# Performance work log

Hardware: AMD Instinct MI355X
Metric: run time of the kernel (lower is better)

The kernel has to match this reference:

```python
import jax, jax.numpy as jnp
import numpy as np

N, B, E = 10000, 4, 160000
C_IN, C_OUT, C_E = 64, 64, 16


def _mk_params(key, c_in, c_out, c_e):
    ks = jax.random.split(key, 8)
    s = 0.1
    return dict(
        w_n=jax.random.normal(ks[0], (c_in, c_out), jnp.float32) * s,
        w_e=jax.random.normal(ks[1], (c_e, c_out), jnp.float32) * s,
        q=jax.random.normal(ks[2], (c_out, c_out), jnp.float32) * s,
        k=jax.random.normal(ks[3], (c_out, c_out), jnp.float32) * s,
        aw=jax.random.normal(ks[4], (3 * c_out, 1), jnp.float32) * s,
        ab=jax.random.normal(ks[5], (1,), jnp.float32) * s,
        ow=jax.random.normal(ks[6], (2 * c_out, c_out), jnp.float32) * s,
        ob=jax.random.normal(ks[7], (c_out,), jnp.float32) * s,
    )


def setup_inputs() -> dict:
    key = jax.random.key(0)
    kx, ke, ka, k1, k2 = jax.random.split(key, 5)
    inp = {
        'X': jax.random.normal(kx, (N, B, C_IN), jnp.float32),
        'edge_index': jax.random.randint(ke, (2, E), 0, N, jnp.int32),
        'edge_attr': jax.random.normal(ka, (E, C_E), jnp.float32),
    }
    p1 = _mk_params(k1, C_IN, C_OUT, C_E)
    p2 = _mk_params(k2, C_OUT, C_OUT, C_E)
    for name, v in p1.items():
        inp[name + '1'] = v
    for name, v in p2.items():
        inp[name + '2'] = v
    return inp


def egnn_conv(x, edge_index, edge_attr, w_n, w_e, q, k, aw, ab, ow, ob, n_nodes):
    # x: [N,B,Cin]; edge_attr: [E,Ce]
    xp = x @ w_n                         # [N,B,C]
    ea = edge_attr @ w_e                 # [E,C]
    src, dst = edge_index[0], edge_index[1]
    xj = xp[src]                         # [E,B,C] gather (source)
    xi = xp[dst]                         # [E,B,C] gather (target)
    qf = xj @ q                          # [E,B,C]
    kf = xi @ k                          # [E,B,C]
    eab = jnp.broadcast_to(ea[:, None, :], qf.shape)  # [E,B,C]
    att_feat = jnp.concatenate([qf, kf, eab], axis=-1)  # [E,B,3C]
    att = jax.nn.sigmoid(att_feat @ aw + ab)            # [E,B,1]
    gate = jax.nn.sigmoid(eab)
    msg = att * xj * gate                # [E,B,C]
    aggr = jax.ops.segment_max(msg, dst, num_segments=n_nodes)  # [N,B,C]
    aggr = jnp.where(jnp.isneginf(aggr), 0.0, aggr)  # empty segments -> 0
    out = jnp.concatenate([xp, aggr], axis=-1) @ ow + ob
    return xp + out


def reference(X, edge_index, edge_attr,
              w_n1, w_e1, q1, k1, aw1, ab1, ow1, ob1,
              w_n2, w_e2, q2, k2, aw2, ab2, ow2, ob2):
    n_nodes = X.shape[0]
    c1 = egnn_conv(X, edge_index, edge_attr, w_n1, w_e1, q1, k1, aw1, ab1, ow1, ob1, n_nodes)
    c1 = jax.nn.leaky_relu(c1, 0.01)
    c2 = egnn_conv(c1, edge_index, edge_attr, w_n2, w_e2, q2, k2, aw2, ab2, ow2, ob2, n_nodes)
    c2 = jax.nn.leaky_relu(c2, 0.01)
    return c2
```

## Files before the change

### kernel.cpp

```cpp
#include <hip/hip_runtime.h>
#include <math.h>

#define NN 10000
#define BB 4
#define EE 160000
#define CC 64
#define CE 16

static constexpr size_t OFF_XPA    = 0;
static constexpr size_t OFF_XPB    = 10240000;
static constexpr size_t OFF_SA     = 20480000;
static constexpr size_t OFF_SB     = 20640000;
static constexpr size_t OFF_VECS   = 20800000;
static constexpr size_t OFF_COUNTS = 20801280;
static constexpr size_t OFF_CURSOR = 20841280;
static constexpr size_t OFF_OFFS   = 20881280;
static constexpr size_t OFF_RECS   = 20921344;
static constexpr size_t OFF_ATT    = 22201344;
static constexpr size_t OFF_SE12   = 24761344;
static constexpr size_t OFF_ORDER  = 26041344;

__device__ __forceinline__ float sigmoidf_(float x) {
    return __builtin_amdgcn_rcpf(1.0f + __expf(-x));
}

__global__ void hist_vecs_kernel(const int* __restrict__ ei, int* __restrict__ counts,
                                 const float* __restrict__ q1, const float* __restrict__ k1,
                                 const float* __restrict__ aw1, const float* __restrict__ we1,
                                 const float* __restrict__ q2, const float* __restrict__ k2,
                                 const float* __restrict__ aw2, const float* __restrict__ we2,
                                 float* __restrict__ vecs) {
    int e = blockIdx.x * blockDim.x + threadIdx.x;
    if (e < EE) atomicAdd(&counts[ei[EE + e]], 1);
    if (blockIdx.x == 0) {
        int t = threadIdx.x;
        if (t < 64) {
            float a = 0.f, b = 0.f, c = 0.f, d = 0.f;
            for (int j = 0; j < 64; ++j) {
                a = fmaf(q1[t * 64 + j], aw1[j], a);
                b = fmaf(k1[t * 64 + j], aw1[64 + j], b);
                c = fmaf(q2[t * 64 + j], aw2[j], c);
                d = fmaf(k2[t * 64 + j], aw2[64 + j], d);
            }
            vecs[t] = a; vecs[64 + t] = b; vecs[144 + t] = c; vecs[208 + t] = d;
        }
        if (t < 16) {
            float a = 0.f, b = 0.f;
            for (int j = 0; j < 64; ++j) {
                a = fmaf(we1[t * 64 + j], aw1[128 + j], a);
                b = fmaf(we2[t * 64 + j], aw2[128 + j], b);
            }
            vecs[128 + t] = a; vecs[272 + t] = b;
        }
    }
}

__global__ __launch_bounds__(1024) void scan_order_kernel(const int* __restrict__ counts,
                                                          int* __restrict__ offs,
                                                          int* __restrict__ order) {
    __shared__ int hist[1024];
    __shared__ int cur[1024];
    __shared__ int startb[1024];
    __shared__ int wsum[16];
    int t = threadIdx.x;
    hist[t] = 0; cur[t] = 0;
    int lane = t & 63, wid = t >> 6;
    int v[10];
    int s = 0;
    #pragma unroll
    for (int j = 0; j < 10; ++j) {
        int i = t * 10 + j;
        v[j] = (i < NN) ? counts[i] : 0;
        s += v[j];
    }
    int ps = s;
    #pragma unroll
    for (int off = 1; off < 64; off <<= 1) {
        int u = __shfl_up(ps, off, 64);
        if (lane >= off) ps += u;
    }
    if (lane == 63) wsum[wid] = ps;
    __syncthreads();
    int wbase = 0;
    for (int w = 0; w < wid; ++w) wbase += wsum[w];
    int tb = wbase + ps - s;
    #pragma unroll
    for (int j = 0; j < 10; ++j) {
        int i = t * 10 + j;
        if (i < NN) offs[i] = tb;
        tb += v[j];
    }
    if (t == 1023) offs[NN] = tb;
    #pragma unroll
    for (int j = 0; j < 10; ++j) {
        int i = t * 10 + j;
        if (i < NN) {
            int d = v[j] > 1023 ? 1023 : v[j];
            atomicAdd(&hist[d], 1);
        }
    }
    __syncthreads();
    int r = 1023 - t;
    int hv = hist[r];
    int ps2 = hv;
    #pragma unroll
    for (int off = 1; off < 64; off <<= 1) {
        int u = __shfl_up(ps2, off, 64);
        if (lane >= off) ps2 += u;
    }
    if (lane == 63) wsum[wid] = ps2;
    __syncthreads();
    int wb2 = 0;
    for (int w = 0; w < wid; ++w) wb2 += wsum[w];
    startb[r] = wb2 + ps2 - hv;
    __syncthreads();
    #pragma unroll
    for (int j = 0; j < 10; ++j) {
        int i = t * 10 + j;
        if (i < NN) {
            int d = v[j] > 1023 ? 1023 : v[j];
            int pos = startb[d] + atomicAdd(&cur[d], 1);
            order[pos] = i;
        }
    }
}

__global__ __launch_bounds__(256) void scatter_kernel(
    const int* __restrict__ ei, const int* __restrict__ offs,
    int* __restrict__ cursor, const float* __restrict__ attr,
    const float* __restrict__ vecs, const float* __restrict__ ab1,
    const float* __restrict__ ab2, int2* __restrict__ recs,
    float2* __restrict__ se12) {
    int e = blockIdx.x * blockDim.x + threadIdx.x;
    if (e >= EE) return;
    int s = ei[e], d = ei[EE + e];
    const float4* ap = (const float4*)(attr + (size_t)e * CE);
    float4 a0 = ap[0], a1 = ap[1], a2 = ap[2], a3 = ap[3];
    const float* v1 = vecs + 128;
    const float* v2 = vecs + 272;
    float s1 = ab1[0], s2 = ab2[0];
    s1 = fmaf(a0.x, v1[0], s1);  s1 = fmaf(a0.y, v1[1], s1);
    s1 = fmaf(a0.z, v1[2], s1);  s1 = fmaf(a0.w, v1[3], s1);
    s1 = fmaf(a1.x, v1[4], s1);  s1 = fmaf(a1.y, v1[5], s1);
    s1 = fmaf(a1.z, v1[6], s1);  s1 = fmaf(a1.w, v1[7], s1);
    s1 = fmaf(a2.x, v1[8], s1);  s1 = fmaf(a2.y, v1[9], s1);
    s1 = fmaf(a2.z, v1[10], s1); s1 = fmaf(a2.w, v1[11], s1);
    s1 = fmaf(a3.x, v1[12], s1); s1 = fmaf(a3.y, v1[13], s1);
    s1 = fmaf(a3.z, v1[14], s1); s1 = fmaf(a3.w, v1[15], s1);
    s2 = fmaf(a0.x, v2[0], s2);  s2 = fmaf(a0.y, v2[1], s2);
    s2 = fmaf(a0.z, v2[2], s2);  s2 = fmaf(a0.w, v2[3], s2);
    s2 = fmaf(a1.x, v2[4], s2);  s2 = fmaf(a1.y, v2[5], s2);
    s2 = fmaf(a1.z, v2[6], s2);  s2 = fmaf(a1.w, v2[7], s2);
    s2 = fmaf(a2.x, v2[8], s2);  s2 = fmaf(a2.y, v2[9], s2);
    s2 = fmaf(a2.z, v2[10], s2); s2 = fmaf(a2.w, v2[11], s2);
    s2 = fmaf(a3.x, v2[12], s2); s2 = fmaf(a3.y, v2[13], s2);
    s2 = fmaf(a3.z, v2[14], s2); s2 = fmaf(a3.w, v2[15], s2);
    int p = atomicAdd(&cursor[d], 1);
    recs[offs[d] + p] = make_int2(s, e);
    se12[e] = make_float2(s1, s2);
}

__global__ __launch_bounds__(256) void node_prep_kernel(
    const float* __restrict__ x, const float* __restrict__ w_n,
    const float* __restrict__ qa, const float* __restrict__ ka,
    float* __restrict__ xp, float* __restrict__ sa, float* __restrict__ sb) {
    __shared__ float w_sh[64 * 64];
    __shared__ float x_sh[4 * BB * CC];
    int t = threadIdx.x;
    for (int i = t; i < 64 * 64; i += 256) w_sh[i] = w_n[i];
    int node0 = blockIdx.x * 4;
    const float4* xg = (const float4*)(x + (size_t)node0 * BB * CC);
    ((float4*)x_sh)[t] = xg[t];
    __syncthreads();
    int wave = t >> 6, lane = t & 63;
    int node = node0 + wave;
    const float* xrow = x_sh + wave * BB * CC;
    float acc0 = 0.f, acc1 = 0.f, acc2 = 0.f, acc3 = 0.f;
    #pragma unroll 8
    for (int ci = 0; ci < 64; ++ci) {
        float w = w_sh[ci * 64 + lane];
        acc0 = fmaf(xrow[ci], w, acc0);
        acc1 = fmaf(xrow[64 + ci], w, acc1);
        acc2 = fmaf(xrow[128 + ci], w, acc2);
        acc3 = fmaf(xrow[192 + ci], w, acc3);
    }
    size_t obase = (size_t)node * BB * CC + lane;
    xp[obase] = acc0;
    xp[obase + 64] = acc1;
    xp[obase + 128] = acc2;
    xp[obase + 192] = acc3;
    float qv = qa[lane], kv = ka[lane];
    float ra0 = acc0 * qv, ra1 = acc1 * qv, ra2 = acc2 * qv, ra3 = acc3 * qv;
    float rb0 = acc0 * kv, rb1 = acc1 * kv, rb2 = acc2 * kv, rb3 = acc3 * kv;
    #pragma unroll
    for (int off = 32; off >= 1; off >>= 1) {
        ra0 += __shfl_xor(ra0, off, 64); ra1 += __shfl_xor(ra1, off, 64);
        ra2 += __shfl_xor(ra2, off, 64); ra3 += __shfl_xor(ra3, off, 64);
        rb0 += __shfl_xor(rb0, off, 64); rb1 += __shfl_xor(rb1, off, 64);
        rb2 += __shfl_xor(rb2, off, 64); rb3 += __shfl_xor(rb3, off, 64);
    }
    if (lane == 0) {
        sa[node * BB + 0] = ra0; sa[node * BB + 1] = ra1;
        sa[node * BB + 2] = ra2; sa[node * BB + 3] = ra3;
        sb[node * BB + 0] = rb0; sb[node * BB + 1] = rb1;
        sb[node * BB + 2] = rb2; sb[node * BB + 3] = rb3;
    }
}

__global__ __launch_bounds__(256) void att_kernel(
    const int* __restrict__ ei, const float2* __restrict__ se12,
    const float* __restrict__ sa, const float* __restrict__ sb,
    float4* __restrict__ att, int sel) {
    int e = blockIdx.x * blockDim.x + threadIdx.x;
    if (e >= EE) return;
    int s = ei[e], d = ei[EE + e];
    float2 se2 = se12[e];
    float se = sel ? se2.y : se2.x;
    float4 sas = *(const float4*)(sa + (size_t)s * BB);
    float4 sbn = *(const float4*)(sb + (size_t)d * BB);
    float4 r;
    r.x = sigmoidf_(sas.x + sbn.x + se);
    r.y = sigmoidf_(sas.y + sbn.y + se);
    r.z = sigmoidf_(sas.z + sbn.z + se);
    r.w = sigmoidf_(sas.w + sbn.w + se);
    att[e] = r;
}

#define FMA4(o_, s_, w_)                                                 \
    o_.x = fmaf(s_, w_.x, o_.x); o_.y = fmaf(s_, w_.y, o_.y);            \
    o_.z = fmaf(s_, w_.z, o_.z); o_.w = fmaf(s_, w_.w, o_.w);

__global__ __launch_bounds__(256) void conv_out_kernel(
    const float* __restrict__ xp,
    const int2* __restrict__ recs,
    const int* __restrict__ offs,
    const float* __restrict__ attr,
    const float* __restrict__ w_e,
    const float4* __restrict__ att,
    const float* __restrict__ ow,
    const float* __restrict__ ob,
    const int* __restrict__ order,
    float* __restrict__ out) {
    __shared__ float aggr_sh[4][BB * 68];
    int t = threadIdx.x;
    int wave = t >> 6, lane = t & 63;
    int node = order[blockIdx.x * 4 + wave];

    float wec[CE];
    #pragma unroll
    for (int j = 0; j < CE; ++j) wec[j] = w_e[j * CC + lane];

    int o0 = offs[node], o1 = offs[node + 1];
    float m0 = -INFINITY, m1 = -INFINITY, m2 = -INFINITY, m3 = -INFINITY;

    int i = o0;
    int2 rec = (i < o1) ? recs[i] : make_int2(0, 0);
    while (i < o1) {
        int2 cur = rec;
        ++i;
        if (i < o1) rec = recs[i];
        int s = cur.x, e = cur.y;
        float4 at = att[e];
        const float4* ap = (const float4*)(attr + (size_t)e * CE);
        float4 a0 = ap[0], a1 = ap[1], a2 = ap[2], a3 = ap[3];
        float g = 0.f;
        g = fmaf(a0.x, wec[0], g);  g = fmaf(a0.y, wec[1], g);
        g = fmaf(a0.z, wec[2], g);  g = fmaf(a0.w, wec[3], g);
        g = fmaf(a1.x, wec[4], g);  g = fmaf(a1.y, wec[5], g);
        g = fmaf(a1.z, wec[6], g);  g = fmaf(a1.w, wec[7], g);
        g = fmaf(a2.x, wec[8], g);  g = fmaf(a2.y, wec[9], g);
        g = fmaf(a2.z, wec[10], g); g = fmaf(a2.w, wec[11], g);
        g = fmaf(a3.x, wec[12], g); g = fmaf(a3.y, wec[13], g);
        g = fmaf(a3.z, wec[14], g); g = fmaf(a3.w, wec[15], g);
        g = sigmoidf_(g);
        const float* xs = xp + (size_t)s * BB * CC + lane;
        float x0 = xs[0], x1 = xs[64], x2 = xs[128], x3 = xs[192];
        m0 = fmaxf(m0, at.x * x0 * g);
        m1 = fmaxf(m1, at.y * x1 * g);
        m2 = fmaxf(m2, at.z * x2 * g);
        m3 = fmaxf(m3, at.w * x3 * g);
    }
    m0 = (m0 == -INFINITY) ? 0.f : m0;
    m1 = (m1 == -INFINITY) ? 0.f : m1;
    m2 = (m2 == -INFINITY) ? 0.f : m2;
    m3 = (m3 == -INFINITY) ? 0.f : m3;

    float* ash = aggr_sh[wave];
    ash[0 * 68 + lane] = m0;
    ash[1 * 68 + lane] = m1;
    ash[2 * 68 + lane] = m2;
    ash[3 * 68 + lane] = m3;
    asm volatile("s_waitcnt lgkmcnt(0)" ::: "memory");
    __builtin_amdgcn_sched_barrier(0);

    int b = lane >> 4, q4 = (lane & 15) << 2;
    const float* agr = ash + b * 68;
    const float* xrow = xp + (size_t)node * (BB * CC) + b * CC;
    const float* owa = ow + q4;
    const float* owb = ow + CC * CC + q4;
    float4 o = make_float4(0.f, 0.f, 0.f, 0.f);
    #pragma unroll 2
    for (int c4 = 0; c4 < 16; ++c4) {
        float4 xv = *(const float4*)(xrow + 4 * c4);
        float4 av = *(const float4*)(agr + 4 * c4);
        const float* wpa = owa + (size_t)(4 * c4) * CC;
        float4 w0 = *(const float4*)(wpa);
        float4 w1 = *(const float4*)(wpa + CC);
        float4 w2 = *(const float4*)(wpa + 2 * CC);
        float4 w3 = *(const float4*)(wpa + 3 * CC);
        const float* wpb = owb + (size_t)(4 * c4) * CC;
        float4 u0 = *(const float4*)(wpb);
        float4 u1 = *(const float4*)(wpb + CC);
        float4 u2 = *(const float4*)(wpb + 2 * CC);
        float4 u3 = *(const float4*)(wpb + 3 * CC);
        FMA4(o, xv.x, w0); FMA4(o, xv.y, w1); FMA4(o, xv.z, w2); FMA4(o, xv.w, w3);
        FMA4(o, av.x, u0); FMA4(o, av.y, u1); FMA4(o, av.z, u2); FMA4(o, av.w, u3);
    }
    float4 xnv = *(const float4*)(xrow + q4);
    float4 ob4 = *(const float4*)(ob + q4);
    float4 r;
    r.x = xnv.x + o.x + ob4.x;
    r.y = xnv.y + o.y + ob4.y;
    r.z = xnv.z + o.z + ob4.z;
    r.w = xnv.w + o.w + ob4.w;
    r.x = (r.x > 0.f) ? r.x : 0.01f * r.x;
    r.y = (r.y > 0.f) ? r.y : 0.01f * r.y;
    r.z = (r.z > 0.f) ? r.z : 0.01f * r.z;
    r.w = (r.w > 0.f) ? r.w : 0.01f * r.w;
    *(float4*)(out + (size_t)node * (BB * CC) + b * CC + q4) = r;
}

extern "C" void kernel_launch(void* const* d_in, const int* in_sizes, int n_in,
                              void* d_out, int out_size, void* d_ws, size_t ws_size,
                              hipStream_t stream) {
    const float* X    = (const float*)d_in[0];
    const int*   ei   = (const int*)d_in[1];
    const float* attr = (const float*)d_in[2];
    const float* w_n1 = (const float*)d_in[3];
    const float* w_e1 = (const float*)d_in[4];
    const float* q1   = (const float*)d_in[5];
    const float* k1   = (const float*)d_in[6];
    const float* aw1  = (const float*)d_in[7];
    const float* ab1  = (const float*)d_in[8];
    const float* ow1  = (const float*)d_in[9];
    const float* ob1  = (const float*)d_in[10];
    const float* w_n2 = (const float*)d_in[11];
    const float* w_e2 = (const float*)d_in[12];
    const float* q2   = (const float*)d_in[13];
    const float* k2   = (const float*)d_in[14];
    const float* aw2  = (const float*)d_in[15];
    const float* ab2  = (const float*)d_in[16];
    const float* ow2  = (const float*)d_in[17];
    const float* ob2  = (const float*)d_in[18];
    float* out = (float*)d_out;

    char* ws = (char*)d_ws;
    float*  xpA    = (float*)(ws + OFF_XPA);
    float*  xpB    = (float*)(ws + OFF_XPB);
    float*  sa     = (float*)(ws + OFF_SA);
    float*  sb     = (float*)(ws + OFF_SB);
    float*  vecs   = (float*)(ws + OFF_VECS);
    int*    counts = (int*)(ws + OFF_COUNTS);
    int*    cursor = (int*)(ws + OFF_CURSOR);
    int*    offs   = (int*)(ws + OFF_OFFS);
    int2*   recs   = (int2*)(ws + OFF_RECS);
    float4* att    = (float4*)(ws + OFF_ATT);
    float2* se12   = (float2*)(ws + OFF_SE12);
    int*    order  = (int*)(ws + OFF_ORDER);

    hipMemsetAsync(counts, 0, 2 * NN * sizeof(int), stream);
    hist_vecs_kernel<<<EE / 256, 256, 0, stream>>>(ei, counts, q1, k1, aw1, w_e1,
                                                   q2, k2, aw2, w_e2, vecs);
    scan_order_kernel<<<1, 1024, 0, stream>>>(counts, offs, order);
    scatter_kernel<<<EE / 256, 256, 0, stream>>>(ei, offs, cursor, attr, vecs,
                                                 ab1, ab2, recs, se12);
    node_prep_kernel<<<NN / 4, 256, 0, stream>>>(X, w_n1, vecs + 0, vecs + 64, xpA, sa, sb);
    att_kernel<<<EE / 256, 256, 0, stream>>>(ei, se12, sa, sb, att, 0);
    conv_out_kernel<<<NN / 4, 256, 0, stream>>>(xpA, recs, offs, attr, w_e1, att,
                                                ow1, ob1, order, xpB);
    node_prep_kernel<<<NN / 4, 256, 0, stream>>>(xpB, w_n2, vecs + 144, vecs + 208, xpA, sa, sb);
    att_kernel<<<EE / 256, 256, 0, stream>>>(ei, se12, sa, sb, att, 1);
    conv_out_kernel<<<NN / 4, 256, 0, stream>>>(xpA, recs, offs, attr, w_e2, att,
                                                ow2, ob2, order, out);
}
```

Before: 336.5 us.

## Split each node across two waves by batch half in conv_out kernel

Each node is now handled by two waves, each covering two of the four batch slots, which doubles the grid size and halves the per-wave edge-loop latency chain. The output projection becomes a per-lane column dot product that reads weights directly from global memory and node features staged in LDS, replacing the float4-tiled matmul. This raises parallelism for the latency-bound gather/max loop, at the cost of computing the edge gate sigmoid and loading edge attributes twice per edge.

After: 357.7 us. +6.3%, slower.

```diff
diff --git a/kernel.cpp b/kernel.cpp
--- a/kernel.cpp
+++ b/kernel.cpp
@@ -226,10 +226,6 @@
     att[e] = r;
 }
 
-#define FMA4(o_, s_, w_)                                                 \
-    o_.x = fmaf(s_, w_.x, o_.x); o_.y = fmaf(s_, w_.y, o_.y);            \
-    o_.z = fmaf(s_, w_.z, o_.z); o_.w = fmaf(s_, w_.w, o_.w);
-
 __global__ __launch_bounds__(256) void conv_out_kernel(
     const float* __restrict__ xp,
     const int2* __restrict__ recs,
@@ -241,17 +237,22 @@
     const float* __restrict__ ob,
     const int* __restrict__ order,
     float* __restrict__ out) {
-    __shared__ float aggr_sh[4][BB * 68];
+    __shared__ float aggr_sh[4][2 * CC];
+    __shared__ float xpn_sh[4][2 * CC];
     int t = threadIdx.x;
     int wave = t >> 6, lane = t & 63;
-    int node = order[blockIdx.x * 4 + wave];
+    int bh = wave & 1;
+    int node = order[blockIdx.x * 2 + (wave >> 1)];
 
     float wec[CE];
     #pragma unroll
     for (int j = 0; j < CE; ++j) wec[j] = w_e[j * CC + lane];
 
+    const float* xn = xp + (size_t)node * BB * CC + bh * 128 + lane;
+    float xn0 = xn[0], xn1 = xn[64];
+
     int o0 = offs[node], o1 = offs[node + 1];
-    float m0 = -INFINITY, m1 = -INFINITY, m2 = -INFINITY, m3 = -INFINITY;
+    float m0 = -INFINITY, m1 = -INFINITY;
 
     int i = o0;
     int2 rec = (i < o1) ? recs[i] : make_int2(0, 0);
@@ -260,7 +261,7 @@
         ++i;
         if (i < o1) rec = recs[i];
         int s = cur.x, e = cur.y;
-        float4 at = att[e];
+        float2 at = ((const float2*)att)[2 * e + bh];
         const float4* ap = (const float4*)(attr + (size_t)e * CE);
         float4 a0 = ap[0], a1 = ap[1], a2 = ap[2], a3 = ap[3];
         float g = 0.f;
@@ -273,61 +274,37 @@
         g = fmaf(a3.x, wec[12], g); g = fmaf(a3.y, wec[13], g);
         g = fmaf(a3.z, wec[14], g); g = fmaf(a3.w, wec[15], g);
         g = sigmoidf_(g);
-        const float* xs = xp + (size_t)s * BB * CC + lane;
-        float x0 = xs[0], x1 = xs[64], x2 = xs[128], x3 = xs[192];
+        const float* xs = xp + (size_t)s * BB * CC + bh * 128 + lane;
+        float x0 = xs[0], x1 = xs[64];
         m0 = fmaxf(m0, at.x * x0 * g);
         m1 = fmaxf(m1, at.y * x1 * g);
-        m2 = fmaxf(m2, at.z * x2 * g);
-        m3 = fmaxf(m3, at.w * x3 * g);
     }
     m0 = (m0 == -INFINITY) ? 0.f : m0;
     m1 = (m1 == -INFINITY) ? 0.f : m1;
-    m2 = (m2 == -INFINITY) ? 0.f : m2;
-    m3 = (m3 == -INFINITY) ? 0.f : m3;
-
-    float* ash = aggr_sh[wave];
-    ash[0 * 68 + lane] = m0;
-    ash[1 * 68 + lane] = m1;
-    ash[2 * 68 + lane] = m2;
-    ash[3 * 68 + lane] = m3;
+
+    float* ag = aggr_sh[wave];
+    float* xq = xpn_sh[wave];
+    ag[lane] = m0; ag[CC + lane] = m1;
+    xq[lane] = xn0; xq[CC + lane] = xn1;
     asm volatile("s_waitcnt lgkmcnt(0)" ::: "memory");
-    __builtin_amdgcn_sched_barrier(0);
-
-    int b = lane >> 4, q4 = (lane & 15) << 2;
-    const float* agr = ash + b * 68;
-    const float* xrow = xp + (size_t)node * (BB * CC) + b * CC;
-    const float* owa = ow + q4;
-    const float* owb = ow + CC * CC + q4;
-    float4 o = make_float4(0.f, 0.f, 0.f, 0.f);
-    #pragma unroll 2
-    for (int c4 = 0; c4 < 16; ++c4) {
-        float4 xv = *(const float4*)(xrow + 4 * c4);
-        float4 av = *(const float4*)(agr + 4 * c4);
-        const float* wpa = owa + (size_t)(4 * c4) * CC;
-        float4 w0 = *(const float4*)(wpa);
-        float4 w1 = *(const float4*)(wpa + CC);
-        float4 w2 = *(const float4*)(wpa + 2 * CC);
-        float4 w3 = *(const float4*)(wpa + 3 * CC);
-        const float* wpb = owb + (size_t)(4 * c4) * CC;
-        float4 u0 = *(const float4*)(wpb);
-        float4 u1 = *(const float4*)(wpb + CC);
-        float4 u2 = *(const float4*)(wpb + 2 * CC);
-        float4 u3 = *(const float4*)(wpb + 3 * CC);
-        FMA4(o, xv.x, w0); FMA4(o, xv.y, w1); FMA4(o, xv.z, w2); FMA4(o, xv.w, w3);
-        FMA4(o, av.x, u0); FMA4(o, av.y, u1); FMA4(o, av.z, u2); FMA4(o, av.w, u3);
-    }
-    float4 xnv = *(const float4*)(xrow + q4);
-    float4 ob4 = *(const float4*)(ob + q4);
-    float4 r;
-    r.x = xnv.x + o.x + ob4.x;
-    r.y = xnv.y + o.y + ob4.y;
-    r.z = xnv.z + o.z + ob4.z;
-    r.w = xnv.w + o.w + ob4.w;
-    r.x = (r.x > 0.f) ? r.x : 0.01f * r.x;
-    r.y = (r.y > 0.f) ? r.y : 0.01f * r.y;
-    r.z = (r.z > 0.f) ? r.z : 0.01f * r.z;
-    r.w = (r.w > 0.f) ? r.w : 0.01f * r.w;
-    *(float4*)(out + (size_t)node * (BB * CC) + b * CC + q4) = r;
+
+    float o0f = 0.f, o1f = 0.f;
+    #pragma unroll 4
+    for (int ci = 0; ci < 64; ++ci) {
+        float wa = ow[ci * 64 + lane];
+        float wb = ow[(64 + ci) * 64 + lane];
+        o0f = fmaf(xq[ci], wa, o0f);
+        o1f = fmaf(xq[CC + ci], wa, o1f);
+        o0f = fmaf(ag[ci], wb, o0f);
+        o1f = fmaf(ag[CC + ci], wb, o1f);
+    }
+    float obv = ob[lane];
+    float r0 = xn0 + o0f + obv;
+    float r1 = xn1 + o1f + obv;
+    r0 = (r0 > 0.f) ? r0 : 0.01f * r0;
+    r1 = (r1 > 0.f) ? r1 : 0.01f * r1;
+    float* op = out + (size_t)node * BB * CC + bh * 128 + lane;
+    op[0] = r0; op[64] = r1;
 }
 
 extern "C" void kernel_launch(void* const* d_in, const int* in_sizes, int n_in,
@@ -376,10 +353,10 @@
                                                  ab1, ab2, recs, se12);
     node_prep_kernel<<<NN / 4, 256, 0, stream>>>(X, w_n1, vecs + 0, vecs + 64, xpA, sa, sb);
     att_kernel<<<EE / 256, 256, 0, stream>>>(ei, se12, sa, sb, att, 0);
-    conv_out_kernel<<<NN / 4, 256, 0, stream>>>(xpA, recs, offs, attr, w_e1, att,
+    conv_out_kernel<<<NN / 2, 256, 0, stream>>>(xpA, recs, offs, attr, w_e1, att,
                                                 ow1, ob1, order, xpB);
     node_prep_kernel<<<NN / 4, 256, 0, stream>>>(xpB, w_n2, vecs + 144, vecs + 208, xpA, sa, sb);
     att_kernel<<<EE / 256, 256, 0, stream>>>(ei, se12, sa, sb, att, 1);
-    conv_out_kernel<<<NN / 4, 256, 0, stream>>>(xpA, recs, offs, attr, w_e2, att,
+    conv_out_kernel<<<NN / 2, 256, 0, stream>>>(xpA, recs, offs, attr, w_e2, att,
                                                 ow2, ob2, order, out);
 }
```
